# Performance work log

Measured on AMD Instinct MI355X. Metric: run time of the kernel, lower is better.

## Reference

```python
import jax, jax.numpy as jnp
import numpy as np

PATCH_GRID = 28          # _embed hard-codes reshape(28, 28, D)
TARGET_HW = (224, 224)   # input_shape[-2:] for RescaleSegmentor


def setup_inputs() -> dict:
    key = jax.random.key(0)
    k1, k2 = jax.random.split(key)
    B = 8
    D = 1536          # 768 (CLS) + 768 (patch token) concat from DINO vitb8
    N_BANK = 50000    # coreset memory bank size
    features = jax.random.normal(k1, (B * PATCH_GRID * PATCH_GRID, D), dtype=jnp.float32)
    memory_bank = jax.random.normal(k2, (N_BANK, D), dtype=jnp.float32)
    return {"features": features, "memory_bank": memory_bank, "batchsize": B}


def reference(features, memory_bank, batchsize):
    # FaissNN IndexFlatL2 with k=1: min squared-L2 distance per query.
    # d2[i,j] = ||q_i||^2 + ||b_j||^2 - 2 q_i . b_j
    qn = jnp.sum(features * features, axis=-1, keepdims=True)          # [Q,1]
    bn = jnp.sum(memory_bank * memory_bank, axis=-1)                   # [N]
    d2 = qn + bn[None, :] - 2.0 * (features @ memory_bank.T)           # [Q,N]
    patch_scores = jnp.min(d2, axis=-1)                                # [Q] (k=1 -> mean of 1 NN)
    # unpatch_scores + PatchMaker.score: max over patches per image
    patch_maps = patch_scores.reshape(batchsize, PATCH_GRID, PATCH_GRID)
    image_scores = jnp.max(patch_maps.reshape(batchsize, -1), axis=-1)  # [B]
    # RescaleSegmentor: bilinear upsample of patch score map to input size
    masks = jax.image.resize(
        patch_maps, (batchsize, TARGET_HW[0], TARGET_HW[1]), method="linear"
    )
    return image_scores, masks
```

## Files before the change

kernel.cpp:

```cpp
#include <hip/hip_runtime.h>
#include <stdint.h>

#define DIM   1536
#define NQ    6272
#define NQP   6400
#define NB    50000
#define NBP2  50176
#define MT2   25
#define NT2   196
#define GRID2 (MT2 * NT2)
#define NKT   24
#define NIT   12
#define NPIX  (8 * 224 * 224)

typedef float f32x4 __attribute__((ext_vector_type(4)));
typedef int   i32x4 __attribute__((ext_vector_type(4)));
typedef __attribute__((address_space(3))) signed char lds_i8;

__device__ inline void gll16(const signed char* g, signed char* l) {
  __builtin_amdgcn_global_load_lds(
      (const __attribute__((address_space(1))) uint32_t*)g,
      (__attribute__((address_space(3))) uint32_t*)l, 16, 0, 0);
}

__global__ void init_kernel(uint32_t* __restrict__ minbits, float* __restrict__ out_scores) {
  int i = blockIdx.x * 256 + threadIdx.x;
  if (i < NQP) minbits[i] = 0x7F800000u;
  if (i < 8)   out_scores[i] = 0.0f;
}

__global__ void quant_rows(const float* __restrict__ src, signed char* __restrict__ dst,
                           float* __restrict__ norms, float* __restrict__ scales,
                           int nsrc, int ndst) {
  int row  = blockIdx.x * 4 + (threadIdx.x >> 6);
  int lane = threadIdx.x & 63;
  if (row >= ndst) return;
  uint32_t* drow = (uint32_t*)(dst + (size_t)row * DIM);
  if (row < nsrc) {
    const float4* s = (const float4*)(src + (size_t)row * DIM);
    float4 v[6]; float ns = 0.f, mx = 0.f;
#pragma unroll
    for (int i = 0; i < 6; ++i) {
      v[i] = s[lane + 64 * i];
      ns += v[i].x * v[i].x + v[i].y * v[i].y + v[i].z * v[i].z + v[i].w * v[i].w;
      mx = fmaxf(mx, fmaxf(fmaxf(fabsf(v[i].x), fabsf(v[i].y)),
                           fmaxf(fabsf(v[i].z), fabsf(v[i].w))));
    }
#pragma unroll
    for (int off = 32; off >= 1; off >>= 1) {
      ns += __shfl_xor(ns, off);
      mx = fmaxf(mx, __shfl_xor(mx, off));
    }
    float inv = (mx > 0.f) ? 127.0f / mx : 0.f;
#pragma unroll
    for (int i = 0; i < 6; ++i) {
      int a = max(-127, min(127, __float2int_rn(v[i].x * inv)));
      int b = max(-127, min(127, __float2int_rn(v[i].y * inv)));
      int c = max(-127, min(127, __float2int_rn(v[i].z * inv)));
      int d = max(-127, min(127, __float2int_rn(v[i].w * inv)));
      drow[lane + 64 * i] = (uint32_t)(a & 255) | ((uint32_t)(b & 255) << 8) |
                            ((uint32_t)(c & 255) << 16) | ((uint32_t)(d & 255) << 24);
    }
    if (lane == 0) { norms[row] = ns; scales[row] = mx * (1.0f / 127.0f); }
  } else {
#pragma unroll
    for (int i = 0; i < 6; ++i) drow[lane + 64 * i] = 0u;
    if (lane == 0) { norms[row] = 1e30f; scales[row] = 0.f; }
  }
}

#define BAR   do { asm volatile("s_barrier" ::: "memory"); \
                   __builtin_amdgcn_sched_barrier(0); } while(0)
#define LGKM(n) do { asm volatile("s_waitcnt lgkmcnt(" #n ")" ::: "memory"); \
                     __builtin_amdgcn_sched_barrier(0); } while(0)
#define VM0   asm volatile("s_waitcnt vmcnt(0)" ::: "memory")
#define VM2   asm volatile("s_waitcnt vmcnt(2)" ::: "memory")
#define VM4   asm volatile("s_waitcnt vmcnt(4)" ::: "memory")
#define PHI   __builtin_amdgcn_s_setprio(1)
#define PLO   __builtin_amdgcn_s_setprio(0)

#define DSR(dst, base, imm) \
  asm volatile("ds_read_b128 %0, %1 offset:%2" : "=v"(dst) : "v"(base), "i"(imm))

#define READ_AQ(dst, bufI, quad) do { \
  DSR(dst[0], aOff, (bufI) * 16384 + (quad) * 4096 + 0);    \
  DSR(dst[1], aOff, (bufI) * 16384 + (quad) * 4096 + 1024); \
  DSR(dst[2], aOff, (bufI) * 16384 + (quad) * 4096 + 2048); \
  DSR(dst[3], aOff, (bufI) * 16384 + (quad) * 4096 + 3072); \
} while(0)

#define READ_B4(dst, bufI) do { \
  DSR(dst[0], bOff, (bufI) * 16384 + 0);    \
  DSR(dst[1], bOff, (bufI) * 16384 + 1024); \
  DSR(dst[2], bOff, (bufI) * 16384 + 2048); \
  DSR(dst[3], bOff, (bufI) * 16384 + 3072); \
} while(0)

#define MFMA8(mb, x0, x1, b4) do { \
  _Pragma("unroll") for (int n_ = 0; n_ < 4; ++n_) { \
    acc[(mb)][n_]     = __builtin_amdgcn_mfma_i32_16x16x64_i8( \
      __builtin_bit_cast(i32x4, (x0)), __builtin_bit_cast(i32x4, b4[n_]), acc[(mb)][n_], 0, 0, 0); \
    acc[(mb) + 1][n_] = __builtin_amdgcn_mfma_i32_16x16x64_i8( \
      __builtin_bit_cast(i32x4, (x1)), __builtin_bit_cast(i32x4, b4[n_]), acc[(mb) + 1][n_], 0, 0, 0); \
  } \
} while(0)

#define STAGE_A(bufI, ktc) do { \
  const signed char* _g = gA + (size_t)srow * DIM + (ktc) + scol; \
  gll16(_g,                      &sA[bufI][sdst]); \
  gll16(_g + (size_t)128 * DIM,  &sA[bufI][8192 + sdst]); \
} while(0)

#define STAGE_B(bufI, ktc) do { \
  const signed char* _g = gB + (size_t)srow * DIM + (ktc) + scol; \
  gll16(_g,                      &sB[bufI][sdst]); \
  gll16(_g + (size_t)128 * DIM,  &sB[bufI][8192 + sdst]); \
} while(0)

#define ITER(T0, SN, RD) do { \
   READ_AQ(aQ, 0, 1); \
    LGKM(4); BAR; PHI; MFMA8(0, aP[0], aP[1], bE); PLO; \
   if (SN) { STAGE_B(0, (T0) + 128); VM2; } else { VM0; } \
    BAR; PHI; MFMA8(2, aP[2], aP[3], bE); PLO; \
   READ_AQ(aP, 1, 0); READ_B4(bO, 1); \
    LGKM(8); BAR; PHI; MFMA8(4, aQ[0], aQ[1], bE); PLO; \
   if (SN) STAGE_A(0, (T0) + 128); \
    BAR; PHI; MFMA8(6, aQ[2], aQ[3], bE); PLO; \
   READ_AQ(aQ, 1, 1); \
    LGKM(4); BAR; PHI; MFMA8(0, aP[0], aP[1], bO); PLO; \
   if (SN) { STAGE_B(1, (T0) + 192); VM2; } \
    BAR; PHI; MFMA8(2, aP[2], aP[3], bO); PLO; \
   if (RD) { READ_AQ(aP, 0, 0); READ_B4(bE, 0); LGKM(8); } else { LGKM(0); } \
    BAR; PHI; MFMA8(4, aQ[0], aQ[1], bO); PLO; \
   if (SN) STAGE_A(1, (T0) + 192); \
    BAR; PHI; MFMA8(6, aQ[2], aQ[3], bO); PLO; \
} while(0)

__global__ __launch_bounds__(512, 2)
void gemm_min8(const signed char* __restrict__ fA, const signed char* __restrict__ bB,
               const float* __restrict__ bn, const float* __restrict__ bscale,
               const float* __restrict__ qscale, uint32_t* __restrict__ minbits) {
  __shared__ __align__(16) signed char sA[2][16384];
  __shared__ __align__(16) signed char sB[2][16384];

  const int nwg = GRID2;
  int bid = blockIdx.x;
  const int qch = nwg >> 3, rch = nwg & 7;
  int xcd = bid & 7, loc = bid >> 3;
  int swz = (xcd < rch ? xcd * (qch + 1) : rch * (qch + 1) + (xcd - rch) * qch) + loc;
  int mt = swz % MT2;
  int nt = swz / MT2;

  int tid = threadIdx.x;
  int lane = tid & 63, wave = tid >> 6;
  int wm = wave >> 2, wn = wave & 3, bq = wn & 1, bh = wn >> 1;
  int lr = lane & 15, k16 = lane >> 4;

  const signed char* gA = fA + (size_t)(mt * 256) * DIM;
  const signed char* gB = bB + (size_t)(nt * 256) * DIM;

  int srow = tid >> 2;
  int scol = ((tid & 3) ^ ((tid >> 3) & 3)) * 16;
  int sdst = tid * 16;

  int cxA = (k16 ^ ((lr >> 1) & 3)) * 16;
  uint32_t aOff = (uint32_t)(uintptr_t)(lds_i8*)&sA[0][(wm * 128 + lr) * 64 + cxA];
  uint32_t bOff = (uint32_t)(uintptr_t)(lds_i8*)&sB[0][(bh * 128 + bq * 64 + lr) * 64 + cxA];

  i32x4 acc[8][4] = {};
  f32x4 aP[4], aQ[4], bE[4], bO[4];

  STAGE_A(0, 0); STAGE_B(0, 0);
  STAGE_A(1, 64); STAGE_B(1, 64);
  VM4; BAR;
  READ_AQ(aP, 0, 0); READ_B4(bE, 0);

#pragma unroll 1
  for (int i = 0; i < NIT - 1; ++i) {
    ITER(i * 128, 1, 1);
  }
  ITER((NIT - 1) * 128, 0, 0);

  float bnv[4], bsv[4];
#pragma unroll
  for (int n_ = 0; n_ < 4; ++n_) {
    int col = nt * 256 + wn * 64 + n_ * 16 + lr;
    bnv[n_] = bn[col];
    bsv[n_] = 2.0f * bscale[col];
  }
  int qbase = mt * 256 + wm * 128;
#pragma unroll
  for (int m_ = 0; m_ < 8; ++m_) {
    f32x4 sq = *(const f32x4*)&qscale[qbase + m_ * 16 + (lane >> 4) * 4];
#pragma unroll
    for (int r = 0; r < 4; ++r) {
      float sqr = sq[r];
      float v =          bnv[0] - bsv[0] * sqr * (float)acc[m_][0][r];
      v = fminf(v, bnv[1] - bsv[1] * sqr * (float)acc[m_][1][r]);
      v = fminf(v, bnv[2] - bsv[2] * sqr * (float)acc[m_][2][r]);
      v = fminf(v, bnv[3] - bsv[3] * sqr * (float)acc[m_][3][r]);
      v = fminf(v, __shfl_xor(v, 1));
      v = fminf(v, __shfl_xor(v, 2));
      v = fminf(v, __shfl_xor(v, 4));
      v = fminf(v, __shfl_xor(v, 8));
      if (lr == 0) {
        int q = qbase + m_ * 16 + (lane >> 4) * 4 + r;
        atomicMin(&minbits[q], __float_as_uint(v));
      }
    }
  }
}

__global__ void scores_kernel(const uint32_t* __restrict__ minbits, const float* __restrict__ qn,
                              float* __restrict__ ps, float* __restrict__ img) {
  int q = blockIdx.x * 256 + threadIdx.x;
  if (q >= NQ) return;
  float s = __uint_as_float(minbits[q]) + qn[q];
  ps[q] = s;
  atomicMax((uint32_t*)&img[q / 784], __float_as_uint(s));
}

__global__ void resize_kernel(const float* __restrict__ ps, float* __restrict__ masks) {
  int idx = blockIdx.x * 256 + threadIdx.x;
  if (idx >= NPIX) return;
  int b   = idx / (224 * 224);
  int rem = idx - b * (224 * 224);
  int oy  = rem / 224;
  int ox  = rem - oy * 224;
  float sy = (oy + 0.5f) * 0.125f - 0.5f;
  float sx = (ox + 0.5f) * 0.125f - 0.5f;
  float fy0 = floorf(sy), fx0 = floorf(sx);
  int y0 = (int)fy0, x0 = (int)fx0;
  float fy = sy - fy0, fx = sx - fx0;
  int y0c = min(max(y0, 0), 27),     y1c = min(max(y0 + 1, 0), 27);
  int x0c = min(max(x0, 0), 27),     x1c = min(max(x0 + 1, 0), 27);
  const float* p = ps + b * 784;
  float top = p[y0c * 28 + x0c] * (1.f - fx) + p[y0c * 28 + x1c] * fx;
  float bot = p[y1c * 28 + x0c] * (1.f - fx) + p[y1c * 28 + x1c] * fx;
  masks[idx] = top * (1.f - fy) + bot * fy;
}

extern "C" void kernel_launch(void* const* d_in, const int* in_sizes, int n_in,
                              void* d_out, int out_size, void* d_ws, size_t ws_size,
                              hipStream_t stream) {
  const float* features = (const float*)d_in[0];
  const float* bank     = (const float*)d_in[1];

  char* ws = (char*)d_ws;
  size_t off = 0;
  signed char* bankQ = (signed char*)(ws + off); off += (size_t)NBP2 * DIM;
  signed char* featQ = (signed char*)(ws + off); off += (size_t)NQP * DIM;
  float*    bn      = (float*)(ws + off);    off += (size_t)NBP2 * 4;
  float*    qn      = (float*)(ws + off);    off += (size_t)NQP * 4;
  float*    bscale  = (float*)(ws + off);    off += (size_t)NBP2 * 4;
  float*    qscale  = (float*)(ws + off);    off += (size_t)NQP * 4;
  uint32_t* minbits = (uint32_t*)(ws + off); off += (size_t)NQP * 4;
  float*    ps      = (float*)(ws + off);    off += (size_t)NQ * 4;

  float* out_scores = (float*)d_out;
  float* masks      = out_scores + 8;

  hipLaunchKernelGGL(init_kernel, dim3(25), dim3(256), 0, stream, minbits, out_scores);
  hipLaunchKernelGGL(quant_rows, dim3(NBP2 / 4), dim3(256), 0, stream, bank, bankQ, bn, bscale, NB, NBP2);
  hipLaunchKernelGGL(quant_rows, dim3(NQP / 4), dim3(256), 0, stream, features, featQ, qn, qscale, NQ, NQP);
  hipLaunchKernelGGL(gemm_min8, dim3(GRID2), dim3(512), 0, stream, featQ, bankQ, bn, bscale, qscale, minbits);
  hipLaunchKernelGGL(scores_kernel, dim3(25), dim3(256), 0, stream, minbits, qn, ps, out_scores);
  hipLaunchKernelGGL(resize_kernel, dim3((NPIX + 255) / 256), dim3(256), 0, stream, ps, masks);
}
```

Baseline: 704.4 us.

## Shrink GEMM tile to 128x256 with triple-buffered LDS and higher occupancy

The int8 GEMM+min kernel moves from 256x256 tiles with double-buffered LDS and 2 blocks per CU to 128x256 tiles with three LDS stages and a launch bound of 4 blocks per CU. Each wave now holds a 64x64 accumulator (4x4 MFMA tiles) instead of 128x64, and the interleaved ping-pong register schedule becomes a simpler two-phase-per-k-step pipeline that waits on all LDS reads each phase. The aim is to raise occupancy and overlap global loads through the deeper LDS pipeline. The cost is more reloads of bank data (twice as many M tiles) and lower MFMA-to-load arithmetic intensity per block.

Result: faster. 662.3 us (-6.0%).

```diff
diff --git a/kernel.cpp b/kernel.cpp
--- a/kernel.cpp
+++ b/kernel.cpp
@@ -6,11 +6,9 @@
 #define NQP   6400
 #define NB    50000
 #define NBP2  50176
-#define MT2   25
-#define NT2   196
-#define GRID2 (MT2 * NT2)
-#define NKT   24
-#define NIT   12
+#define MT3   50
+#define NT3   196
+#define GRID3 (MT3 * NT3)
 #define NPIX  (8 * 224 * 224)
 
 typedef float f32x4 __attribute__((ext_vector_type(4)));
@@ -71,115 +69,91 @@
 
 #define BAR   do { asm volatile("s_barrier" ::: "memory"); \
                    __builtin_amdgcn_sched_barrier(0); } while(0)
-#define LGKM(n) do { asm volatile("s_waitcnt lgkmcnt(" #n ")" ::: "memory"); \
-                     __builtin_amdgcn_sched_barrier(0); } while(0)
+#define LGKM0 do { asm volatile("s_waitcnt lgkmcnt(0)" ::: "memory"); \
+                   __builtin_amdgcn_sched_barrier(0); } while(0)
 #define VM0   asm volatile("s_waitcnt vmcnt(0)" ::: "memory")
-#define VM2   asm volatile("s_waitcnt vmcnt(2)" ::: "memory")
-#define VM4   asm volatile("s_waitcnt vmcnt(4)" ::: "memory")
+#define VM3   asm volatile("s_waitcnt vmcnt(3)" ::: "memory")
 #define PHI   __builtin_amdgcn_s_setprio(1)
 #define PLO   __builtin_amdgcn_s_setprio(0)
 
 #define DSR(dst, base, imm) \
   asm volatile("ds_read_b128 %0, %1 offset:%2" : "=v"(dst) : "v"(base), "i"(imm))
 
-#define READ_AQ(dst, bufI, quad) do { \
-  DSR(dst[0], aOff, (bufI) * 16384 + (quad) * 4096 + 0);    \
-  DSR(dst[1], aOff, (bufI) * 16384 + (quad) * 4096 + 1024); \
-  DSR(dst[2], aOff, (bufI) * 16384 + (quad) * 4096 + 2048); \
-  DSR(dst[3], aOff, (bufI) * 16384 + (quad) * 4096 + 3072); \
-} while(0)
-
-#define READ_B4(dst, bufI) do { \
-  DSR(dst[0], bOff, (bufI) * 16384 + 0);    \
-  DSR(dst[1], bOff, (bufI) * 16384 + 1024); \
-  DSR(dst[2], bOff, (bufI) * 16384 + 2048); \
-  DSR(dst[3], bOff, (bufI) * 16384 + 3072); \
-} while(0)
-
-#define MFMA8(mb, x0, x1, b4) do { \
-  _Pragma("unroll") for (int n_ = 0; n_ < 4; ++n_) { \
-    acc[(mb)][n_]     = __builtin_amdgcn_mfma_i32_16x16x64_i8( \
-      __builtin_bit_cast(i32x4, (x0)), __builtin_bit_cast(i32x4, b4[n_]), acc[(mb)][n_], 0, 0, 0); \
-    acc[(mb) + 1][n_] = __builtin_amdgcn_mfma_i32_16x16x64_i8( \
-      __builtin_bit_cast(i32x4, (x1)), __builtin_bit_cast(i32x4, b4[n_]), acc[(mb) + 1][n_], 0, 0, 0); \
-  } \
-} while(0)
-
-#define STAGE_A(bufI, ktc) do { \
-  const signed char* _g = gA + (size_t)srow * DIM + (ktc) + scol; \
-  gll16(_g,                      &sA[bufI][sdst]); \
-  gll16(_g + (size_t)128 * DIM,  &sA[bufI][8192 + sdst]); \
-} while(0)
-
-#define STAGE_B(bufI, ktc) do { \
-  const signed char* _g = gB + (size_t)srow * DIM + (ktc) + scol; \
-  gll16(_g,                      &sB[bufI][sdst]); \
-  gll16(_g + (size_t)128 * DIM,  &sB[bufI][8192 + sdst]); \
-} while(0)
-
-#define ITER(T0, SN, RD) do { \
-   READ_AQ(aQ, 0, 1); \
-    LGKM(4); BAR; PHI; MFMA8(0, aP[0], aP[1], bE); PLO; \
-   if (SN) { STAGE_B(0, (T0) + 128); VM2; } else { VM0; } \
-    BAR; PHI; MFMA8(2, aP[2], aP[3], bE); PLO; \
-   READ_AQ(aP, 1, 0); READ_B4(bO, 1); \
-    LGKM(8); BAR; PHI; MFMA8(4, aQ[0], aQ[1], bE); PLO; \
-   if (SN) STAGE_A(0, (T0) + 128); \
-    BAR; PHI; MFMA8(6, aQ[2], aQ[3], bE); PLO; \
-   READ_AQ(aQ, 1, 1); \
-    LGKM(4); BAR; PHI; MFMA8(0, aP[0], aP[1], bO); PLO; \
-   if (SN) { STAGE_B(1, (T0) + 192); VM2; } \
-    BAR; PHI; MFMA8(2, aP[2], aP[3], bO); PLO; \
-   if (RD) { READ_AQ(aP, 0, 0); READ_B4(bE, 0); LGKM(8); } else { LGKM(0); } \
-    BAR; PHI; MFMA8(4, aQ[0], aQ[1], bO); PLO; \
-   if (SN) STAGE_A(1, (T0) + 192); \
-    BAR; PHI; MFMA8(6, aQ[2], aQ[3], bO); PLO; \
-} while(0)
-
-__global__ __launch_bounds__(512, 2)
+#define MFMA8N(nb, bb) do { \
+  _Pragma("unroll") for (int m_ = 0; m_ < 4; ++m_) \
+  _Pragma("unroll") for (int n_ = 0; n_ < 2; ++n_) \
+    acc[m_][(nb) + n_] = __builtin_amdgcn_mfma_i32_16x16x64_i8( \
+      __builtin_bit_cast(i32x4, a[m_]), __builtin_bit_cast(i32x4, bb[n_]), \
+      acc[m_][(nb) + n_], 0, 0, 0); \
+} while(0)
+
+#define STAGE_AB(sb, ktc) do { \
+  gll16(gA + gOffA + (ktc), &sA[sb][sdst]); \
+  const signed char* _g = gB + gOffA + (ktc); \
+  gll16(_g,                      &sB[sb][sdst]); \
+  gll16(_g + (size_t)128 * DIM,  &sB[sb][8192 + sdst]); \
+} while(0)
+
+#define PH_A(buf, SN, sb, ktc) do { \
+  DSR(a[0], aOff, (buf) * 8192 + 0);    DSR(a[1], aOff, (buf) * 8192 + 1024); \
+  DSR(a[2], aOff, (buf) * 8192 + 2048); DSR(a[3], aOff, (buf) * 8192 + 3072); \
+  DSR(b01[0], bOff, (buf) * 16384 + 0); DSR(b01[1], bOff, (buf) * 16384 + 1024); \
+  if (SN) STAGE_AB(sb, ktc); \
+  LGKM0; BAR; PHI; MFMA8N(0, b01); PLO; \
+} while(0)
+
+#define PH_B(buf, GATE) do { \
+  DSR(b23[0], bOff, (buf) * 16384 + 2048); DSR(b23[1], bOff, (buf) * 16384 + 3072); \
+  LGKM0; GATE; BAR; PHI; MFMA8N(2, b23); PLO; \
+} while(0)
+
+__global__ __launch_bounds__(512, 4)
 void gemm_min8(const signed char* __restrict__ fA, const signed char* __restrict__ bB,
                const float* __restrict__ bn, const float* __restrict__ bscale,
                const float* __restrict__ qscale, uint32_t* __restrict__ minbits) {
-  __shared__ __align__(16) signed char sA[2][16384];
-  __shared__ __align__(16) signed char sB[2][16384];
-
-  const int nwg = GRID2;
+  __shared__ __align__(16) signed char sA[3][8192];
+  __shared__ __align__(16) signed char sB[3][16384];
+
+  const int nwg = GRID3;
   int bid = blockIdx.x;
   const int qch = nwg >> 3, rch = nwg & 7;
   int xcd = bid & 7, loc = bid >> 3;
   int swz = (xcd < rch ? xcd * (qch + 1) : rch * (qch + 1) + (xcd - rch) * qch) + loc;
-  int mt = swz % MT2;
-  int nt = swz / MT2;
+  int mt = swz % MT3;
+  int nt = swz / MT3;
 
   int tid = threadIdx.x;
   int lane = tid & 63, wave = tid >> 6;
-  int wm = wave >> 2, wn = wave & 3, bq = wn & 1, bh = wn >> 1;
+  int wm = wave >> 2, wn = wave & 3;
   int lr = lane & 15, k16 = lane >> 4;
 
-  const signed char* gA = fA + (size_t)(mt * 256) * DIM;
+  const signed char* gA = fA + (size_t)(mt * 128) * DIM;
   const signed char* gB = bB + (size_t)(nt * 256) * DIM;
 
-  int srow = tid >> 2;
-  int scol = ((tid & 3) ^ ((tid >> 3) & 3)) * 16;
+  size_t gOffA = (size_t)(tid >> 2) * DIM + ((tid & 3) ^ ((tid >> 3) & 3)) * 16;
   int sdst = tid * 16;
 
   int cxA = (k16 ^ ((lr >> 1) & 3)) * 16;
-  uint32_t aOff = (uint32_t)(uintptr_t)(lds_i8*)&sA[0][(wm * 128 + lr) * 64 + cxA];
-  uint32_t bOff = (uint32_t)(uintptr_t)(lds_i8*)&sB[0][(bh * 128 + bq * 64 + lr) * 64 + cxA];
-
-  i32x4 acc[8][4] = {};
-  f32x4 aP[4], aQ[4], bE[4], bO[4];
-
-  STAGE_A(0, 0); STAGE_B(0, 0);
-  STAGE_A(1, 64); STAGE_B(1, 64);
-  VM4; BAR;
-  READ_AQ(aP, 0, 0); READ_B4(bE, 0);
+  uint32_t aOff = (uint32_t)(uintptr_t)(lds_i8*)&sA[0][(wm * 64 + lr) * 64 + cxA];
+  uint32_t bOff = (uint32_t)(uintptr_t)(lds_i8*)&sB[0][(wn * 64 + lr) * 64 + cxA];
+
+  i32x4 acc[4][4] = {};
+  f32x4 a[4], b01[2], b23[2];
+
+  STAGE_AB(0, 0);
+  STAGE_AB(1, 64);
+  VM3; BAR;
 
 #pragma unroll 1
-  for (int i = 0; i < NIT - 1; ++i) {
-    ITER(i * 128, 1, 1);
-  }
-  ITER((NIT - 1) * 128, 0, 0);
+  for (int j = 0; j < 7; ++j) {
+    int kb = j * 192;
+    PH_A(0, 1, 2, kb + 128); PH_B(0, VM3);
+    PH_A(1, 1, 0, kb + 192); PH_B(1, VM3);
+    PH_A(2, 1, 1, kb + 256); PH_B(2, VM3);
+  }
+  PH_A(0, 1, 2, 1472); PH_B(0, VM3);
+  PH_A(1, 0, 0, 0);    PH_B(1, VM0);
+  PH_A(2, 0, 0, 0);    PH_B(2, ;);
 
   float bnv[4], bsv[4];
 #pragma unroll
@@ -188,9 +162,9 @@
     bnv[n_] = bn[col];
     bsv[n_] = 2.0f * bscale[col];
   }
-  int qbase = mt * 256 + wm * 128;
-#pragma unroll
-  for (int m_ = 0; m_ < 8; ++m_) {
+  int qbase = mt * 128 + wm * 64;
+#pragma unroll
+  for (int m_ = 0; m_ < 4; ++m_) {
     f32x4 sq = *(const f32x4*)&qscale[qbase + m_ * 16 + (lane >> 4) * 4];
 #pragma unroll
     for (int r = 0; r < 4; ++r) {
@@ -263,7 +237,7 @@
   hipLaunchKernelGGL(init_kernel, dim3(25), dim3(256), 0, stream, minbits, out_scores);
   hipLaunchKernelGGL(quant_rows, dim3(NBP2 / 4), dim3(256), 0, stream, bank, bankQ, bn, bscale, NB, NBP2);
   hipLaunchKernelGGL(quant_rows, dim3(NQP / 4), dim3(256), 0, stream, features, featQ, qn, qscale, NQ, NQP);
-  hipLaunchKernelGGL(gemm_min8, dim3(GRID2), dim3(512), 0, stream, featQ, bankQ, bn, bscale, qscale, minbits);
+  hipLaunchKernelGGL(gemm_min8, dim3(GRID3), dim3(512), 0, stream, featQ, bankQ, bn, bscale, qscale, minbits);
   hipLaunchKernelGGL(scores_kernel, dim3(25), dim3(256), 0, stream, minbits, qn, ps, out_scores);
   hipLaunchKernelGGL(resize_kernel, dim3((NPIX + 255) / 256), dim3(256), 0, stream, ps, masks);
 }
```
